# Optimization experiments

Measured on AMD Instinct MI355X. Metric: run time of the kernel, lower is better.

The kernel has to match this reference:

```python
import jax, jax.numpy as jnp
import numpy as np

N_NODES = 50000
N_EDGES = 1600000
D_FEAT = 48


def setup_inputs() -> dict:
    key = jax.random.key(0)
    k1, k2, k3, k4, k5 = jax.random.split(key, 5)
    return {
        "x": jax.random.normal(k1, (N_EDGES, D_FEAT), dtype=jnp.float32),
        "switch": jax.random.uniform(k2, (N_EDGES,), dtype=jnp.float32),
        "edge_src": jax.random.randint(k3, (N_EDGES,), 0, N_NODES, dtype=jnp.int32),
        "edge_dst": jax.random.randint(k4, (N_EDGES,), 0, N_NODES, dtype=jnp.int32),
        "species": jax.random.randint(k5, (N_NODES,), 0, 100, dtype=jnp.int32),
    }


def reference(x, switch, edge_src, edge_dst, species):
    # nat = number of atoms, taken from species shape (static)
    nat = species.shape[0]
    # apply_switch: multiply per-edge switch into edge features [E, D] * [E, 1]
    xw = x * switch[:, None]
    # scatter-add edges to source atoms
    out = jax.ops.segment_sum(xw, edge_src, num_segments=nat)
    # antisymmetric: subtract scatter-add to destination atoms
    out = out - jax.ops.segment_sum(xw, edge_dst, num_segments=nat)
    return out  # [nat, D]
```

## Files before the change

### kernel.cpp

```cpp
#include <hip/hip_runtime.h>
#include <hip/hip_bf16.h>
#include <math.h>


#define D_FEAT 48
#define RNODES 64
#define RSHIFT 6
#define NB_MAX 1024
#define EPB 4096
#define SORT_CAP 8192

__global__ __launch_bounds__(256) void hist_kernel(
        const int* __restrict__ src, const int* __restrict__ dst,
        int* __restrict__ gcnt, int E, int NB) {
    __shared__ int lh[NB_MAX];
    for (int b = threadIdx.x; b < NB; b += 256) lh[b] = 0;
    __syncthreads();
    int t = threadIdx.x;
    int base = blockIdx.x * EPB;
    #pragma unroll
    for (int i = 0; i < EPB / 1024; ++i) {
        int e = base + i * 1024 + t * 4;
        if (e + 3 < E) {
            int4 s4 = *(const int4*)(src + e);
            int4 d4 = *(const int4*)(dst + e);
            atomicAdd(&lh[s4.x >> RSHIFT], 1);
            atomicAdd(&lh[s4.y >> RSHIFT], 1);
            atomicAdd(&lh[s4.z >> RSHIFT], 1);
            atomicAdd(&lh[s4.w >> RSHIFT], 1);
            atomicAdd(&lh[d4.x >> RSHIFT], 1);
            atomicAdd(&lh[d4.y >> RSHIFT], 1);
            atomicAdd(&lh[d4.z >> RSHIFT], 1);
            atomicAdd(&lh[d4.w >> RSHIFT], 1);
        } else {
            for (int j = 0; j < 4; ++j) {
                int ee = e + j;
                if (ee < E) {
                    atomicAdd(&lh[src[ee] >> RSHIFT], 1);
                    atomicAdd(&lh[dst[ee] >> RSHIFT], 1);
                }
            }
        }
    }
    __syncthreads();
    for (int b = threadIdx.x; b < NB; b += 256) {
        int c = lh[b];
        if (c) atomicAdd(&gcnt[b], c);
    }
}

__global__ __launch_bounds__(1024) void scan_kernel(
        const int* __restrict__ gcnt, int* __restrict__ goff,
        int* __restrict__ gcur, int* __restrict__ noff,
        int NB, int N, int total) {
    __shared__ int s[NB_MAX];
    int t = threadIdx.x;
    int v = (t < NB) ? gcnt[t] : 0;
    s[t] = v;
    __syncthreads();
    for (int d = 1; d < 1024; d <<= 1) {
        int a = (t >= d) ? s[t - d] : 0;
        __syncthreads();
        s[t] += a;
        __syncthreads();
    }
    if (t < NB) {
        int excl = s[t] - v;
        goff[t] = excl;
        gcur[t] = excl;
    }
    if (t == 0) {
        goff[NB] = total;
        noff[N] = total;
    }
}

__device__ __forceinline__ void bin_place(int e, int node, int side,
                                          int* lh, const int* lbase,
                                          int* __restrict__ items) {
    int b = node >> RSHIFT;
    int p = lbase[b] + atomicAdd(&lh[b], 1);
    items[p] = (e << 7) | (side << 6) | (node & (RNODES - 1));
}

__global__ __launch_bounds__(256) void bin_kernel(
        const int* __restrict__ src, const int* __restrict__ dst,
        int* __restrict__ gcur, int* __restrict__ items, int E, int NB) {
    __shared__ int lh[NB_MAX];
    __shared__ int lbase[NB_MAX];
    for (int b = threadIdx.x; b < NB; b += 256) lh[b] = 0;
    __syncthreads();
    int t = threadIdx.x;
    int base = blockIdx.x * EPB;
    #pragma unroll
    for (int i = 0; i < EPB / 1024; ++i) {
        int e = base + i * 1024 + t * 4;
        if (e + 3 < E) {
            int4 s4 = *(const int4*)(src + e);
            int4 d4 = *(const int4*)(dst + e);
            atomicAdd(&lh[s4.x >> RSHIFT], 1);
            atomicAdd(&lh[s4.y >> RSHIFT], 1);
            atomicAdd(&lh[s4.z >> RSHIFT], 1);
            atomicAdd(&lh[s4.w >> RSHIFT], 1);
            atomicAdd(&lh[d4.x >> RSHIFT], 1);
            atomicAdd(&lh[d4.y >> RSHIFT], 1);
            atomicAdd(&lh[d4.z >> RSHIFT], 1);
            atomicAdd(&lh[d4.w >> RSHIFT], 1);
        } else {
            for (int j = 0; j < 4; ++j) {
                int ee = e + j;
                if (ee < E) {
                    atomicAdd(&lh[src[ee] >> RSHIFT], 1);
                    atomicAdd(&lh[dst[ee] >> RSHIFT], 1);
                }
            }
        }
    }
    __syncthreads();
    for (int b = threadIdx.x; b < NB; b += 256) {
        int c = lh[b];
        lbase[b] = c ? atomicAdd(&gcur[b], c) : 0;
        lh[b] = 0;
    }
    __syncthreads();
    #pragma unroll
    for (int i = 0; i < EPB / 1024; ++i) {
        int e = base + i * 1024 + t * 4;
        if (e + 3 < E) {
            int4 s4 = *(const int4*)(src + e);
            int4 d4 = *(const int4*)(dst + e);
            bin_place(e + 0, s4.x, 0, lh, lbase, items);
            bin_place(e + 1, s4.y, 0, lh, lbase, items);
            bin_place(e + 2, s4.z, 0, lh, lbase, items);
            bin_place(e + 3, s4.w, 0, lh, lbase, items);
            bin_place(e + 0, d4.x, 1, lh, lbase, items);
            bin_place(e + 1, d4.y, 1, lh, lbase, items);
            bin_place(e + 2, d4.z, 1, lh, lbase, items);
            bin_place(e + 3, d4.w, 1, lh, lbase, items);
        } else {
            for (int j = 0; j < 4; ++j) {
                int ee = e + j;
                if (ee < E) {
                    bin_place(ee, src[ee], 0, lh, lbase, items);
                    bin_place(ee, dst[ee], 1, lh, lbase, items);
                }
            }
        }
    }
}

__global__ __launch_bounds__(256) void sort_kernel(
        int* __restrict__ items, const int* __restrict__ goff,
        int* __restrict__ noff, int N) {
    __shared__ int sitems[SORT_CAP];
    __shared__ int ccnt[RNODES];
    __shared__ int cbase[RNODES];
    int r = blockIdx.x;
    int lo = goff[r], hi = goff[r + 1];
    int cnt = hi - lo;
    int t = threadIdx.x;

    if (t < RNODES) ccnt[t] = 0;
    __syncthreads();
    #pragma unroll 4
    for (int i = t; i < cnt; i += 256) {
        int it = items[lo + i];
        sitems[i] = it;
        atomicAdd(&ccnt[it & (RNODES - 1)], 1);
    }
    __syncthreads();
    if (t < RNODES) {
        int c = ccnt[t];
        int v = c;
        #pragma unroll
        for (int d = 1; d < 64; d <<= 1) {
            int a = __shfl_up(v, d);
            if (t >= d) v += a;
        }
        int excl = v - c;
        cbase[t] = excl;
        int n = r * RNODES + t;
        if (n < N) noff[n] = lo + excl;
        ccnt[t] = 0;
    }
    __syncthreads();
    #pragma unroll 4
    for (int i = t; i < cnt; i += 256) {
        int it = sitems[i];
        int loc = it & (RNODES - 1);
        int p = cbase[loc] + atomicAdd(&ccnt[loc], 1);
        items[lo + p] = it;
    }
}

__global__ __launch_bounds__(256, 4) void gather_kernel(
        const float4* __restrict__ x4, const float* __restrict__ sw,
        const int* __restrict__ noff, const int* __restrict__ items,
        float* __restrict__ out, int N) {
    int n = (blockIdx.x * blockDim.x + threadIdx.x) >> 6;
    int lane = threadIdx.x & 63;
    if (n >= N) return;

    int lo = noff[n], hi = noff[n + 1];
    int cnt = hi - lo;
    int grp = lane >> 4;
    int sub = lane & 15;

    float4 acc = make_float4(0.f, 0.f, 0.f, 0.f);

    for (int cb = 0; cb < cnt; cb += 64) {
        int chunk = items[lo + min(cb + lane, cnt - 1)];
        int rem = cnt - cb;
        #pragma unroll
        for (int k = 0; k < 16; ++k) {
            int idx = k * 4 + grp;
            int it = __shfl(chunk, idx);
            int e = it >> 7;
            float w = (idx < rem) ? sw[e] : 0.f;
            w = (it & RNODES) ? -w : w;
            if (sub < 12) {
                float4 v = x4[(size_t)e * 12 + sub];
                acc.x += w * v.x;
                acc.y += w * v.y;
                acc.z += w * v.z;
                acc.w += w * v.w;
            }
        }
    }

    acc.x += __shfl_down(acc.x, 32);
    acc.y += __shfl_down(acc.y, 32);
    acc.z += __shfl_down(acc.z, 32);
    acc.w += __shfl_down(acc.w, 32);
    acc.x += __shfl_down(acc.x, 16);
    acc.y += __shfl_down(acc.y, 16);
    acc.z += __shfl_down(acc.z, 16);
    acc.w += __shfl_down(acc.w, 16);

    if (lane < 12) {
        float4* orow = (float4*)(out + (size_t)n * D_FEAT);
        orow[lane] = acc;
    }
}

#define TPE 12
__global__ void atomic_fallback_kernel(const float4* __restrict__ x,
                                       const float* __restrict__ sw,
                                       const int* __restrict__ src,
                                       const int* __restrict__ dst,
                                       float* __restrict__ out, int n_edges) {
    int g = blockIdx.x * blockDim.x + threadIdx.x;
    int e = g / TPE;
    int q = g - e * TPE;
    if (e >= n_edges) return;
    float s = sw[e];
    float4 v = x[(size_t)e * TPE + q];
    v.x *= s; v.y *= s; v.z *= s; v.w *= s;
    int si = src[e], di = dst[e];
    float* po = out + (size_t)si * D_FEAT + q * 4;
    unsafeAtomicAdd(po + 0, v.x);
    unsafeAtomicAdd(po + 1, v.y);
    unsafeAtomicAdd(po + 2, v.z);
    unsafeAtomicAdd(po + 3, v.w);
    float* pd = out + (size_t)di * D_FEAT + q * 4;
    unsafeAtomicAdd(pd + 0, -v.x);
    unsafeAtomicAdd(pd + 1, -v.y);
    unsafeAtomicAdd(pd + 2, -v.z);
    unsafeAtomicAdd(pd + 3, -v.w);
}

extern "C" void kernel_launch(void* const* d_in, const int* in_sizes, int n_in,
                              void* d_out, int out_size, void* d_ws, size_t ws_size,
                              hipStream_t stream) {
    const float* x  = (const float*)d_in[0];
    const float* sw = (const float*)d_in[1];
    const int*   src = (const int*)d_in[2];
    const int*   dst = (const int*)d_in[3];
    float* out = (float*)d_out;

    int E = in_sizes[1];
    int N = in_sizes[4];
    int NB = (N + RNODES - 1) / RNODES;

    size_t need = ((size_t)NB * 3 + 1 + (size_t)N + 1 + 2 * (size_t)E) * sizeof(int);

    int mean = (NB > 0) ? (int)((long long)2 * E / NB) : 0;
    bool bucket_risk = mean + 16 * (int)sqrtf((float)(mean > 0 ? mean : 1)) > SORT_CAP;

    if (NB > NB_MAX || ws_size < need || bucket_risk) {
        hipMemsetAsync(d_out, 0, (size_t)out_size * sizeof(float), stream);
        long long total = (long long)E * TPE;
        int grid = (int)((total + 255) / 256);
        atomic_fallback_kernel<<<grid, 256, 0, stream>>>(
            (const float4*)x, sw, src, dst, out, E);
        return;
    }

    int* gcnt  = (int*)d_ws;
    int* goff  = gcnt + NB;
    int* gcur  = goff + NB + 1;
    int* noff  = gcur + NB;
    int* items = noff + N + 1;

    hipMemsetAsync(gcnt, 0, (size_t)NB * sizeof(int), stream);

    int eblk = (E + EPB - 1) / EPB;
    hist_kernel<<<eblk, 256, 0, stream>>>(src, dst, gcnt, E, NB);
    scan_kernel<<<1, 1024, 0, stream>>>(gcnt, goff, gcur, noff, NB, N, 2 * E);
    bin_kernel<<<eblk, 256, 0, stream>>>(src, dst, gcur, items, E, NB);
    sort_kernel<<<NB, 256, 0, stream>>>(items, goff, noff, N);

    int gblk = (int)(((long long)N * 64 + 255) / 256);
    gather_kernel<<<gblk, 256, 0, stream>>>((const float4*)x, sw, noff, items, out, N);
}
```

Baseline: 581.7 us.

## Pre-scale edge features into fp16 buffer and gather from half-precision copy

Adds a convert pass that multiplies each edge row by its switch value and stores it as fp16 in workspace. A new gather kernel reads these 96-byte rows instead of the 192-byte fp32 rows and applies the sign by XOR on the half bits. This halves the bytes moved by the random gather, at the cost of an extra streaming pass over x (read fp32, write fp16). It also introduces fp16 rounding error in the summed output, which could break tolerance.

```diff
diff --git a/kernel.cpp b/kernel.cpp
--- a/kernel.cpp
+++ b/kernel.cpp
@@ -1,5 +1,6 @@
 #include <hip/hip_runtime.h>
 #include <hip/hip_bf16.h>
+#include <hip/hip_fp16.h>
 #include <math.h>
 
 
@@ -9,6 +10,28 @@
 #define NB_MAX 1024
 #define EPB 4096
 #define SORT_CAP 8192
+
+__global__ __launch_bounds__(256) void convert_kernel(
+        const float4* __restrict__ x4, const float* __restrict__ sw,
+        uint4* __restrict__ xwh, int G) {
+    int g = blockIdx.x * 256 + threadIdx.x;
+    if (g >= G) return;
+    unsigned ug = (unsigned)g;
+    int e = (int)(ug / 6u);
+    float s = sw[e];
+    const float4* p = x4 + (size_t)g * 2;
+    float4 a = p[0], b = p[1];
+    __half2 h0 = __floats2half2_rn(a.x * s, a.y * s);
+    __half2 h1 = __floats2half2_rn(a.z * s, a.w * s);
+    __half2 h2 = __floats2half2_rn(b.x * s, b.y * s);
+    __half2 h3 = __floats2half2_rn(b.z * s, b.w * s);
+    uint4 o;
+    o.x = __builtin_bit_cast(unsigned int, h0);
+    o.y = __builtin_bit_cast(unsigned int, h1);
+    o.z = __builtin_bit_cast(unsigned int, h2);
+    o.w = __builtin_bit_cast(unsigned int, h3);
+    xwh[g] = o;
+}
 
 __global__ __launch_bounds__(256) void hist_kernel(
         const int* __restrict__ src, const int* __restrict__ dst,
@@ -193,6 +216,60 @@
     }
 }
 
+__global__ __launch_bounds__(256, 8) void gather_f16_kernel(
+        const uint4* __restrict__ xwh, const int* __restrict__ noff,
+        const int* __restrict__ items, float* __restrict__ out, int N) {
+    int n = (blockIdx.x * blockDim.x + threadIdx.x) >> 6;
+    int lane = threadIdx.x & 63;
+    if (n >= N) return;
+
+    int lo = noff[n], hi = noff[n + 1];
+    int cnt = hi - lo;
+    int grp = lane >> 3;
+    int sub = lane & 7;
+
+    float4 acc0 = make_float4(0.f, 0.f, 0.f, 0.f);
+    float4 acc1 = make_float4(0.f, 0.f, 0.f, 0.f);
+
+    for (int cb = 0; cb < cnt; cb += 64) {
+        int chunk = items[lo + min(cb + lane, cnt - 1)];
+        int rem = cnt - cb;
+        #pragma unroll
+        for (int k = 0; k < 8; ++k) {
+            int idx = k * 8 + grp;
+            int it = __shfl(chunk, idx);
+            if (idx < rem && sub < 6) {
+                uint4 q = xwh[(size_t)(it >> 7) * 6 + sub];
+                unsigned m = (it & RNODES) ? 0x80008000u : 0u;
+                float2 f0 = __half22float2(__builtin_bit_cast(__half2, q.x ^ m));
+                float2 f1 = __half22float2(__builtin_bit_cast(__half2, q.y ^ m));
+                float2 f2 = __half22float2(__builtin_bit_cast(__half2, q.z ^ m));
+                float2 f3 = __half22float2(__builtin_bit_cast(__half2, q.w ^ m));
+                acc0.x += f0.x; acc0.y += f0.y; acc0.z += f1.x; acc0.w += f1.y;
+                acc1.x += f2.x; acc1.y += f2.y; acc1.z += f3.x; acc1.w += f3.y;
+            }
+        }
+    }
+
+    #pragma unroll
+    for (int d = 32; d >= 8; d >>= 1) {
+        acc0.x += __shfl_down(acc0.x, d);
+        acc0.y += __shfl_down(acc0.y, d);
+        acc0.z += __shfl_down(acc0.z, d);
+        acc0.w += __shfl_down(acc0.w, d);
+        acc1.x += __shfl_down(acc1.x, d);
+        acc1.y += __shfl_down(acc1.y, d);
+        acc1.z += __shfl_down(acc1.z, d);
+        acc1.w += __shfl_down(acc1.w, d);
+    }
+
+    if (lane < 6) {
+        float4* orow = (float4*)(out + (size_t)n * D_FEAT);
+        orow[lane * 2 + 0] = acc0;
+        orow[lane * 2 + 1] = acc1;
+    }
+}
+
 __global__ __launch_bounds__(256, 4) void gather_kernel(
         const float4* __restrict__ x4, const float* __restrict__ sw,
         const int* __restrict__ noff, const int* __restrict__ items,
@@ -282,12 +359,15 @@
     int N = in_sizes[4];
     int NB = (N + RNODES - 1) / RNODES;
 
-    size_t need = ((size_t)NB * 3 + 1 + (size_t)N + 1 + 2 * (size_t)E) * sizeof(int);
+    size_t xwh_bytes = (size_t)E * D_FEAT * 2;
+    size_t need_int  = ((size_t)NB * 3 + 1 + (size_t)N + 1 + 2 * (size_t)E)
+                       * sizeof(int);
+    size_t need_f16  = xwh_bytes + need_int;
 
     int mean = (NB > 0) ? (int)((long long)2 * E / NB) : 0;
     bool bucket_risk = mean + 16 * (int)sqrtf((float)(mean > 0 ? mean : 1)) > SORT_CAP;
 
-    if (NB > NB_MAX || ws_size < need || bucket_risk) {
+    if (NB > NB_MAX || ws_size < need_int || bucket_risk) {
         hipMemsetAsync(d_out, 0, (size_t)out_size * sizeof(float), stream);
         long long total = (long long)E * TPE;
         int grid = (int)((total + 255) / 256);
@@ -296,13 +376,24 @@
         return;
     }
 
-    int* gcnt  = (int*)d_ws;
+    bool use_f16 = (ws_size >= need_f16);
+    char* base = (char*)d_ws;
+    uint4* xwh = (uint4*)base;
+    int* ints  = (int*)(use_f16 ? (base + xwh_bytes) : base);
+
+    int* gcnt  = ints;
     int* goff  = gcnt + NB;
     int* gcur  = goff + NB + 1;
     int* noff  = gcur + NB;
     int* items = noff + N + 1;
 
     hipMemsetAsync(gcnt, 0, (size_t)NB * sizeof(int), stream);
+
+    if (use_f16) {
+        int G = E * (D_FEAT / 8);
+        int cblk = (G + 255) / 256;
+        convert_kernel<<<cblk, 256, 0, stream>>>((const float4*)x, sw, xwh, G);
+    }
 
     int eblk = (E + EPB - 1) / EPB;
     hist_kernel<<<eblk, 256, 0, stream>>>(src, dst, gcnt, E, NB);
@@ -311,5 +402,11 @@
     sort_kernel<<<NB, 256, 0, stream>>>(items, goff, noff, N);
 
     int gblk = (int)(((long long)N * 64 + 255) / 256);
-    gather_kernel<<<gblk, 256, 0, stream>>>((const float4*)x, sw, noff, items, out, N);
-}
+    if (use_f16) {
+        gather_f16_kernel<<<gblk, 256, 0, stream>>>(
+            (const uint4*)xwh, noff, items, out, N);
+    } else {
+        gather_kernel<<<gblk, 256, 0, stream>>>(
+            (const float4*)x, sw, noff, items, out, N);
+    }
+}
```

After: 590.9 us. No clear change (+1.6%).
